# Kernel optimization log

Measured on AMD Instinct MI355X. Metric: run time of the kernel, lower is better.

## Reference

```python
import jax, jax.numpy as jnp
import numpy as np

B, S, E, H = 8, 2048, 512, 8
DH = E // H
NEG = -1e30


def setup_inputs() -> dict:
    key = jax.random.key(0)
    ks = jax.random.split(key, 6)
    return {
        "x": jax.random.normal(ks[0], (B, S, E), dtype=jnp.float32),
        "W_qkv": jax.random.normal(ks[1], (E, 3 * E), dtype=jnp.float32) * 0.02,
        "b_qkv": jax.random.normal(ks[2], (3 * E,), dtype=jnp.float32) * 0.02,
        "W_out": jax.random.normal(ks[3], (E, E), dtype=jnp.float32) * 0.02,
        "b_out": jax.random.normal(ks[4], (E,), dtype=jnp.float32) * 0.02,
        "rel_pos": jax.random.normal(ks[5], (1, H, S, S), dtype=jnp.float32) * 0.02,
    }


def reference(x, W_qkv, b_qkv, W_out, b_out, rel_pos):
    b, s, e = x.shape
    scale = DH ** -0.5
    qkv = x @ W_qkv + b_qkv                     # [b, s, 3e]
    qkv = qkv.reshape(b, s, 3, H, DH)
    q = jnp.transpose(qkv[:, :, 0], (0, 2, 1, 3))  # [b, h, s, dh]
    k = jnp.transpose(qkv[:, :, 1], (0, 2, 1, 3))
    v = jnp.transpose(qkv[:, :, 2], (0, 2, 1, 3))
    scores = jnp.einsum("bhqd,bhkd->bhqk", q, k) * scale
    scores = scores + rel_pos[:, :, :s, :s]
    causal = jnp.tril(jnp.ones((s, s), dtype=bool))
    scores = jnp.where(causal[None, None], scores, NEG)
    attn = jax.nn.softmax(scores, axis=-1)
    out = jnp.einsum("bhqk,bhkd->bhqd", attn, v)  # [b, h, s, dh]
    out = jnp.transpose(out, (0, 2, 1, 3)).reshape(b, s, e)
    return out @ W_out + b_out
```

## Files before the change

kernel.cpp:

```cpp
#include <hip/hip_runtime.h>
#include <cstdint>


#define DEVI __device__ __forceinline__

typedef __bf16 bf8 __attribute__((ext_vector_type(8)));
typedef float f4 __attribute__((ext_vector_type(4)));
typedef unsigned short us8 __attribute__((ext_vector_type(8)));
typedef unsigned short us4 __attribute__((ext_vector_type(4)));

typedef const unsigned int __attribute__((address_space(1))) gu32;
typedef unsigned int __attribute__((address_space(3))) lu32;

DEVI unsigned short f2bf(float f) {
  unsigned u = __builtin_bit_cast(unsigned, f);
  u += 0x7fffu + ((u >> 16) & 1u);
  return (unsigned short)(u >> 16);
}

DEVI void gl_lds16(const void* g, void* l) {
  __builtin_amdgcn_global_load_lds((gu32*)g, (lu32*)l, 16, 0, 0);
}

DEVI bf8 comb(us4 a, us4 b) {
  us8 r;
  r[0]=a[0]; r[1]=a[1]; r[2]=a[2]; r[3]=a[3];
  r[4]=b[0]; r[5]=b[1]; r[6]=b[2]; r[7]=b[3];
  return __builtin_bit_cast(bf8, r);
}

__global__ __launch_bounds__(256) void k_convert_x(const float* __restrict__ x,
                                                   unsigned short* __restrict__ xb) {
  int c = blockIdx.x * 256 + threadIdx.x;
  int row = c >> 6, cl = c & 63;
  const float* s = x + ((size_t)row << 9) + (cl << 3);
  float4 a = *(const float4*)s;
  float4 b = *(const float4*)(s + 4);
  us8 o;
  o[0]=f2bf(a.x); o[1]=f2bf(a.y); o[2]=f2bf(a.z); o[3]=f2bf(a.w);
  o[4]=f2bf(b.x); o[5]=f2bf(b.y); o[6]=f2bf(b.z); o[7]=f2bf(b.w);
  int p = (cl & ~7) | ((cl & 7) ^ (row & 7));
  *(us8*)(xb + ((size_t)row << 9) + (p << 3)) = o;
}

__global__ __launch_bounds__(256) void k_transpose_w(const float* __restrict__ W,
                                                     unsigned short* __restrict__ Wt, int N) {
  __shared__ float t[32][33];
  int k0 = blockIdx.x * 32, n0 = blockIdx.y * 32;
  int tx = threadIdx.x & 31, ty = threadIdx.x >> 5;
#pragma unroll
  for (int r = 0; r < 4; ++r)
    t[ty + r * 8][tx] = W[(size_t)(k0 + ty + r * 8) * N + n0 + tx];
  __syncthreads();
#pragma unroll
  for (int r = 0; r < 4; ++r) {
    int n = n0 + ty + r * 8, k = k0 + tx;
    int k2 = (k & ~63) | ((((k >> 3) & 7) ^ (n & 7)) << 3) | (k & 7);
    Wt[((size_t)n << 9) + k2] = f2bf(t[tx][ty + r * 8]);
  }
}

template <int EPI>
__global__ __launch_bounds__(256, 2)
void k_gemm(const unsigned short* __restrict__ Ag, const unsigned short* __restrict__ Bg,
            const float* __restrict__ bias, float* __restrict__ Of,
            unsigned short* __restrict__ Oq, unsigned short* __restrict__ Ok,
            unsigned short* __restrict__ Ov) {
  __shared__ __align__(16) unsigned short lds[128 * 64 * 2];
  unsigned short* Al = lds;
  unsigned short* Bl = lds + 128 * 64;
  const int tid = threadIdx.x, wv = tid >> 6, lane = tid & 63, g = lane >> 4, cl = lane & 15;
  const int wm = wv >> 1, wn = wv & 1;
  const int row0 = blockIdx.x * 128, col0 = blockIdx.y * 128;
  f4 acc[4][4];
#pragma unroll
  for (int i = 0; i < 4; ++i)
#pragma unroll
    for (int j = 0; j < 4; ++j) acc[i][j] = (f4){0.f, 0.f, 0.f, 0.f};

  for (int kt = 0; kt < 8; ++kt) {
#pragma unroll
    for (int j = 0; j < 4; ++j) {
      int ci = wv * 4 + j;
      int gci = ci * 64 + lane;
      int r = gci >> 3, cc = gci & 7;
      gl_lds16(Ag + ((size_t)(row0 + r) << 9) + kt * 64 + cc * 8, Al + ci * 512);
      gl_lds16(Bg + ((size_t)(col0 + r) << 9) + kt * 64 + cc * 8, Bl + ci * 512);
    }
    __syncthreads();
#pragma unroll
    for (int kk = 0; kk < 2; ++kk) {
      bf8 af[4], bb[4];
#pragma unroll
      for (int mf = 0; mf < 4; ++mf) {
        int r = wm * 64 + mf * 16 + cl;
        int cc = (kk * 4 + g) ^ (r & 7);
        af[mf] = *(const bf8*)(Al + r * 64 + cc * 8);
      }
#pragma unroll
      for (int nf = 0; nf < 4; ++nf) {
        int r = wn * 64 + nf * 16 + cl;
        int cc = (kk * 4 + g) ^ (r & 7);
        bb[nf] = *(const bf8*)(Bl + r * 64 + cc * 8);
      }
#pragma unroll
      for (int mf = 0; mf < 4; ++mf)
#pragma unroll
        for (int nf = 0; nf < 4; ++nf)
          acc[mf][nf] = __builtin_amdgcn_mfma_f32_16x16x32_bf16(af[mf], bb[nf], acc[mf][nf], 0, 0, 0);
    }
    __syncthreads();
  }

  if (EPI == 1) {
#pragma unroll
    for (int nf = 0; nf < 4; ++nf) {
      int col = col0 + wn * 64 + nf * 16 + cl;
      float bv = bias[col];
#pragma unroll
      for (int mf = 0; mf < 4; ++mf) {
#pragma unroll
        for (int j = 0; j < 4; ++j) {
          int row = row0 + wm * 64 + mf * 16 + 4 * g + j;
          Of[((size_t)row << 9) + col] = acc[mf][nf][j] + bv;
        }
      }
    }
  } else {
    const int which = col0 >> 9;
#pragma unroll
    for (int nf = 0; nf < 4; ++nf) {
      int col = col0 + wn * 64 + nf * 16 + cl;
      float bv = bias[col];
      int d = col & 63, h = (col >> 6) & 7;
#pragma unroll
      for (int mf = 0; mf < 4; ++mf) {
        int row = row0 + wm * 64 + mf * 16 + 4 * g;
        int b = row >> 11, s = row & 2047;
        size_t fb = ((size_t)b * 8 + h) * 131072;
        if (which == 0) {
#pragma unroll
          for (int j = 0; j < 4; ++j) {
            int ss = s + j;
            size_t off = fb + (size_t)((ss >> 4) * 1024 + (d >> 5) * 512 +
                                       (((d >> 3) & 3) * 16 + (ss & 15)) * 8 + (d & 7));
            Oq[off] = f2bf((acc[mf][nf][j] + bv) * 0.125f);
          }
        } else if (which == 1) {
#pragma unroll
          for (int j = 0; j < 4; ++j) {
            int ss = s + j;
            size_t off = fb + (size_t)((ss >> 6) * 4096 + (d >> 5) * 2048 + ((ss >> 4) & 3) * 512 +
                                       (((d >> 3) & 3) * 16 + (ss & 15)) * 8 + (d & 7));
            Ok[off] = f2bf(acc[mf][nf][j] + bv);
          }
        } else {
          us4 o;
#pragma unroll
          for (int j = 0; j < 4; ++j) o[j] = f2bf(acc[mf][nf][j] + bv);
          size_t off = fb + (size_t)((s >> 6) * 4096 + ((s >> 5) & 1) * 2048 + (d >> 4) * 512 +
                                     ((((s >> 3) & 3) * 16) + (d & 15)) * 8 + (s & 7));
          *(us4*)(Ov + off) = o;
        }
      }
    }
  }
}

__global__ __launch_bounds__(256, 3)
void k_attn(const unsigned short* __restrict__ Qf, const unsigned short* __restrict__ Kf,
            const unsigned short* __restrict__ Vf, const float* __restrict__ rel,
            unsigned short* __restrict__ AO) {
  __shared__ __align__(16) unsigned short Pl[4][16 * 68];
  const int tid = threadIdx.x, wv = tid >> 6, lane = tid & 63, g = lane >> 4, cl = lane & 15;
  int bid = blockIdx.x;
  int glo = bid & 7, rest = bid >> 3;
  int b = rest & 7, ghi = rest >> 3;
  int grp = ghi * 8 + glo;
  int h = grp >> 5, qt = 31 - (grp & 31);
  int qb = qt << 6;
  size_t fb = (((size_t)b << 3) + h) * 131072;
  const unsigned short* Qp = Qf + fb;
  const unsigned short* Kp = Kf + fb;
  const unsigned short* Vp = Vf + fb;
  const float* relp = rel + ((size_t)h << 22);
  const int qrb = qb + wv * 16;
  const int q16 = (qt << 2) + wv;

  bf8 qf[2];
#pragma unroll
  for (int kk = 0; kk < 2; ++kk)
    qf[kk] = *(const bf8*)(Qp + q16 * 1024 + kk * 512 + lane * 8);

  f4 oa[4];
  float mrun[4], lrun[4];
#pragma unroll
  for (int j = 0; j < 4; ++j) { mrun[j] = -1e30f; lrun[j] = 0.f; }
#pragma unroll
  for (int ct = 0; ct < 4; ++ct) oa[ct] = (f4){0.f, 0.f, 0.f, 0.f};

  unsigned short* pw = Pl[wv];

  for (int kt = 0; kt <= qt; ++kt) {
    int kb = kt << 6;
    const unsigned short* Kt = Kp + kt * 4096;
    const unsigned short* Vt = Vp + kt * 4096;
    bf8 kf[2][4], vf[2][4];
#pragma unroll
    for (int kk = 0; kk < 2; ++kk)
#pragma unroll
      for (int ct = 0; ct < 4; ++ct) {
        kf[kk][ct] = *(const bf8*)(Kt + kk * 2048 + ct * 512 + lane * 8);
        vf[kk][ct] = *(const bf8*)(Vt + kk * 2048 + ct * 512 + lane * 8);
      }
    float rl[4][4];
    const float* rb = relp + ((size_t)(qrb + 4 * g) << 11) + kb + cl;
#pragma unroll
    for (int ct = 0; ct < 4; ++ct)
#pragma unroll
      for (int j = 0; j < 4; ++j)
        rl[ct][j] = rb[(j << 11) + ct * 16];

    f4 sa[4];
#pragma unroll
    for (int ct = 0; ct < 4; ++ct) sa[ct] = (f4){0.f, 0.f, 0.f, 0.f};
#pragma unroll
    for (int kk = 0; kk < 2; ++kk)
#pragma unroll
      for (int ct = 0; ct < 4; ++ct)
        sa[ct] = __builtin_amdgcn_mfma_f32_16x16x32_bf16(qf[kk], kf[kk][ct], sa[ct], 0, 0, 0);

    if (kt == qt) {
#pragma unroll
      for (int ct = 0; ct < 4; ++ct) {
        int kcol = kb + ct * 16 + cl;
#pragma unroll
        for (int j = 0; j < 4; ++j) {
          int qrow = qrb + 4 * g + j;
          float sv = sa[ct][j] + rl[ct][j];
          sa[ct][j] = (kcol > qrow) ? -1e30f : sv;
        }
      }
    } else {
#pragma unroll
      for (int ct = 0; ct < 4; ++ct)
#pragma unroll
        for (int j = 0; j < 4; ++j) sa[ct][j] += rl[ct][j];
    }
    float al[4], mx[4];
#pragma unroll
    for (int j = 0; j < 4; ++j) {
      float m0 = fmaxf(fmaxf(sa[0][j], sa[1][j]), fmaxf(sa[2][j], sa[3][j]));
      m0 = fmaxf(m0, __shfl_xor(m0, 1, 16));
      m0 = fmaxf(m0, __shfl_xor(m0, 2, 16));
      m0 = fmaxf(m0, __shfl_xor(m0, 4, 16));
      m0 = fmaxf(m0, __shfl_xor(m0, 8, 16));
      float mn = fmaxf(mrun[j], m0);
      al[j] = __expf(mrun[j] - mn);
      mrun[j] = mn;
      mx[j] = mn;
    }
#pragma unroll
    for (int ct = 0; ct < 4; ++ct)
#pragma unroll
      for (int j = 0; j < 4; ++j) sa[ct][j] = __expf(sa[ct][j] - mx[j]);
#pragma unroll
    for (int j = 0; j < 4; ++j) {
      float rs = sa[0][j] + sa[1][j] + sa[2][j] + sa[3][j];
      rs += __shfl_xor(rs, 1, 16);
      rs += __shfl_xor(rs, 2, 16);
      rs += __shfl_xor(rs, 4, 16);
      rs += __shfl_xor(rs, 8, 16);
      lrun[j] = lrun[j] * al[j] + rs;
    }
#pragma unroll
    for (int ct = 0; ct < 4; ++ct) {
      oa[ct][0] *= al[0]; oa[ct][1] *= al[1]; oa[ct][2] *= al[2]; oa[ct][3] *= al[3];
    }
#pragma unroll
    for (int ct = 0; ct < 4; ++ct)
#pragma unroll
      for (int j = 0; j < 4; ++j)
        pw[(4 * g + j) * 68 + ct * 16 + cl] = f2bf(sa[ct][j]);
#pragma unroll
    for (int kk = 0; kk < 2; ++kk) {
      us4 p0 = *(const us4*)(pw + cl * 68 + kk * 32 + g * 8);
      us4 p1 = *(const us4*)(pw + cl * 68 + kk * 32 + g * 8 + 4);
      bf8 pf = comb(p0, p1);
#pragma unroll
      for (int ct = 0; ct < 4; ++ct)
        oa[ct] = __builtin_amdgcn_mfma_f32_16x16x32_bf16(pf, vf[kk][ct], oa[ct], 0, 0, 0);
    }
  }
#pragma unroll
  for (int j = 0; j < 4; ++j) {
    float inv = 1.0f / lrun[j];
    int s = qrb + 4 * g + j;
#pragma unroll
    for (int ct = 0; ct < 4; ++ct) {
      int d = ct * 16 + cl;
      int d2 = (d & 7) | (((d >> 3) ^ (s & 7)) << 3);
      AO[(((size_t)b << 11) + s) * 512 + h * 64 + d2] = f2bf(oa[ct][j] * inv);
    }
  }
}

extern "C" void kernel_launch(void* const* d_in, const int* in_sizes, int n_in,
                              void* d_out, int out_size, void* d_ws, size_t ws_size,
                              hipStream_t stream) {
  const float* x    = (const float*)d_in[0];
  const float* Wqkv = (const float*)d_in[1];
  const float* bqkv = (const float*)d_in[2];
  const float* Wout = (const float*)d_in[3];
  const float* bout = (const float*)d_in[4];
  const float* rel  = (const float*)d_in[5];
  float* out = (float*)d_out;

  unsigned short* Qw  = (unsigned short*)d_ws;
  unsigned short* Kw  = Qw  + 8388608;
  unsigned short* Vw  = Kw  + 8388608;
  unsigned short* AOw = Vw  + 8388608;
  unsigned short* Xb  = AOw + 8388608;
  unsigned short* WtQ = Xb  + 8388608;
  unsigned short* WtO = WtQ + 786432;

  k_convert_x<<<dim3(4096), dim3(256), 0, stream>>>(x, Xb);
  k_transpose_w<<<dim3(16, 48), dim3(256), 0, stream>>>(Wqkv, WtQ, 1536);
  k_transpose_w<<<dim3(16, 16), dim3(256), 0, stream>>>(Wout, WtO, 512);
  k_gemm<0><<<dim3(128, 12), dim3(256), 0, stream>>>(Xb, WtQ, bqkv, nullptr, Qw, Kw, Vw);
  k_attn<<<dim3(2048), dim3(256), 0, stream>>>(Qw, Kw, Vw, rel, AOw);
  k_gemm<1><<<dim3(128, 4), dim3(256), 0, stream>>>(AOw, WtO, bout, out, nullptr, nullptr, nullptr);
}
```

Baseline: 243.1 us.

## Process two query tiles per block sharing K/V loads; prelayout rel_pos as bf16

```diff
diff --git a/kernel.cpp b/kernel.cpp
--- a/kernel.cpp
+++ b/kernel.cpp
@@ -58,6 +58,21 @@
     int k2 = (k & ~63) | ((((k >> 3) & 7) ^ (n & 7)) << 3) | (k & 7);
     Wt[((size_t)n << 9) + k2] = f2bf(t[tx][ty + r * 8]);
   }
+}
+
+__global__ __launch_bounds__(256) void k_relconv(const float* __restrict__ rel,
+                                                 unsigned short* __restrict__ relt) {
+  int t = blockIdx.x * 256 + threadIdx.x;
+  int lane = t & 63, ct = (t >> 6) & 3, kt = (t >> 8) & 31, q16 = (t >> 13) & 127, h = t >> 20;
+  if (kt > (q16 >> 2)) return;
+  int row0 = (q16 << 4) + ((lane >> 4) << 2);
+  int col = (kt << 6) + (ct << 4) + (lane & 15);
+  const float* rp = rel + ((size_t)h << 22) + ((size_t)row0 << 11) + col;
+  us4 o;
+#pragma unroll
+  for (int j = 0; j < 4; ++j) o[j] = f2bf(rp[(size_t)j << 11]);
+  size_t idx = ((((((size_t)h << 7) | q16) << 5) | kt) << 2 | ct) << 6 | lane;
+  *(us4*)(relt + (idx << 2)) = o;
 }
 
 template <int EPI>
@@ -167,140 +182,169 @@
   }
 }
 
+DEVI void qk16(f4* sa, const bf8* qf_, const bf8 kf[2][4]) {
+#pragma unroll
+  for (int ct = 0; ct < 4; ++ct) sa[ct] = (f4){0.f, 0.f, 0.f, 0.f};
+#pragma unroll
+  for (int kk = 0; kk < 2; ++kk)
+#pragma unroll
+    for (int ct = 0; ct < 4; ++ct)
+      sa[ct] = __builtin_amdgcn_mfma_f32_16x16x32_bf16(qf_[kk], kf[kk][ct], sa[ct], 0, 0, 0);
+}
+
+template <bool RELT>
+DEVI void addrel16(f4* sa, const float* relp, const unsigned short* relt,
+                   int h, int q16X, int rX, int kt, int kb, int g, int cl, int lane) {
+  if constexpr (RELT) {
+    const unsigned short* tb = relt + (((((size_t)h << 7) | q16X) << 5) | kt) * 1024;
+#pragma unroll
+    for (int ct = 0; ct < 4; ++ct) {
+      us4 r = *(const us4*)(tb + ((ct << 6) | lane) * 4);
+#pragma unroll
+      for (int j = 0; j < 4; ++j)
+        sa[ct][j] += __builtin_bit_cast(float, (unsigned)r[j] << 16);
+    }
+  } else {
+    const float* rb = relp + ((size_t)(rX + 4 * g) << 11) + kb + cl;
+#pragma unroll
+    for (int ct = 0; ct < 4; ++ct)
+#pragma unroll
+      for (int j = 0; j < 4; ++j) sa[ct][j] += rb[((size_t)j << 11) + ct * 16];
+  }
+}
+
+DEVI void maskdiag(f4* sa, int rX, int kb, int g, int cl) {
+#pragma unroll
+  for (int ct = 0; ct < 4; ++ct) {
+    int kcol = kb + ct * 16 + cl;
+#pragma unroll
+    for (int j = 0; j < 4; ++j)
+      if (kcol > rX + 4 * g + j) sa[ct][j] = -1e30f;
+  }
+}
+
+DEVI void smpv16(f4* sa, f4* oa, float* mr, float* lr, const bf8 vf[2][4],
+                 unsigned short* pw, int g, int cl) {
+  float al[4], mx[4];
+#pragma unroll
+  for (int j = 0; j < 4; ++j) {
+    float m0 = fmaxf(fmaxf(sa[0][j], sa[1][j]), fmaxf(sa[2][j], sa[3][j]));
+    m0 = fmaxf(m0, __shfl_xor(m0, 1, 16));
+    m0 = fmaxf(m0, __shfl_xor(m0, 2, 16));
+    m0 = fmaxf(m0, __shfl_xor(m0, 4, 16));
+    m0 = fmaxf(m0, __shfl_xor(m0, 8, 16));
+    float mn = fmaxf(mr[j], m0);
+    al[j] = __expf(mr[j] - mn);
+    mr[j] = mn; mx[j] = mn;
+  }
+#pragma unroll
+  for (int ct = 0; ct < 4; ++ct)
+#pragma unroll
+    for (int j = 0; j < 4; ++j) sa[ct][j] = __expf(sa[ct][j] - mx[j]);
+#pragma unroll
+  for (int j = 0; j < 4; ++j) {
+    float rs = sa[0][j] + sa[1][j] + sa[2][j] + sa[3][j];
+    rs += __shfl_xor(rs, 1, 16);
+    rs += __shfl_xor(rs, 2, 16);
+    rs += __shfl_xor(rs, 4, 16);
+    rs += __shfl_xor(rs, 8, 16);
+    lr[j] = lr[j] * al[j] + rs;
+  }
+#pragma unroll
+  for (int ct = 0; ct < 4; ++ct) {
+    oa[ct][0] *= al[0]; oa[ct][1] *= al[1]; oa[ct][2] *= al[2]; oa[ct][3] *= al[3];
+  }
+#pragma unroll
+  for (int ct = 0; ct < 4; ++ct)
+#pragma unroll
+    for (int j = 0; j < 4; ++j)
+      pw[(4 * g + j) * 68 + ct * 16 + cl] = f2bf(sa[ct][j]);
+#pragma unroll
+  for (int kk = 0; kk < 2; ++kk) {
+    us4 p0 = *(const us4*)(pw + cl * 68 + kk * 32 + g * 8);
+    us4 p1 = *(const us4*)(pw + cl * 68 + kk * 32 + g * 8 + 4);
+    bf8 pf = comb(p0, p1);
+#pragma unroll
+    for (int ct = 0; ct < 4; ++ct)
+      oa[ct] = __builtin_amdgcn_mfma_f32_16x16x32_bf16(pf, vf[kk][ct], oa[ct], 0, 0, 0);
+  }
+}
+
+template <bool RELT>
 __global__ __launch_bounds__(256, 3)
 void k_attn(const unsigned short* __restrict__ Qf, const unsigned short* __restrict__ Kf,
             const unsigned short* __restrict__ Vf, const float* __restrict__ rel,
-            unsigned short* __restrict__ AO) {
+            const unsigned short* __restrict__ relt, unsigned short* __restrict__ AO) {
   __shared__ __align__(16) unsigned short Pl[4][16 * 68];
   const int tid = threadIdx.x, wv = tid >> 6, lane = tid & 63, g = lane >> 4, cl = lane & 15;
   int bid = blockIdx.x;
   int glo = bid & 7, rest = bid >> 3;
   int b = rest & 7, ghi = rest >> 3;
   int grp = ghi * 8 + glo;
-  int h = grp >> 5, qt = 31 - (grp & 31);
-  int qb = qt << 6;
+  int h = grp >> 4, qt2 = 15 - (grp & 15);
+  int qb2 = qt2 << 7;
   size_t fb = (((size_t)b << 3) + h) * 131072;
   const unsigned short* Qp = Qf + fb;
   const unsigned short* Kp = Kf + fb;
   const unsigned short* Vp = Vf + fb;
   const float* relp = rel + ((size_t)h << 22);
-  const int qrb = qb + wv * 16;
-  const int q16 = (qt << 2) + wv;
-
-  bf8 qf[2];
-#pragma unroll
-  for (int kk = 0; kk < 2; ++kk)
-    qf[kk] = *(const bf8*)(Qp + q16 * 1024 + kk * 512 + lane * 8);
-
-  f4 oa[4];
-  float mrun[4], lrun[4];
-#pragma unroll
-  for (int j = 0; j < 4; ++j) { mrun[j] = -1e30f; lrun[j] = 0.f; }
-#pragma unroll
-  for (int ct = 0; ct < 4; ++ct) oa[ct] = (f4){0.f, 0.f, 0.f, 0.f};
+  const int rA = qb2 + wv * 16, rB = rA + 64;
+  const int q16A = (qt2 << 3) + wv, q16B = q16A + 4;
+
+  bf8 qfA[2], qfB[2];
+#pragma unroll
+  for (int kk = 0; kk < 2; ++kk) {
+    qfA[kk] = *(const bf8*)(Qp + q16A * 1024 + kk * 512 + lane * 8);
+    qfB[kk] = *(const bf8*)(Qp + q16B * 1024 + kk * 512 + lane * 8);
+  }
+
+  f4 oaA[4], oaB[4];
+  float mA[4], lA[4], mB[4], lB[4];
+#pragma unroll
+  for (int j = 0; j < 4; ++j) { mA[j] = -1e30f; lA[j] = 0.f; mB[j] = -1e30f; lB[j] = 0.f; }
+#pragma unroll
+  for (int ct = 0; ct < 4; ++ct) { oaA[ct] = (f4){0.f,0.f,0.f,0.f}; oaB[ct] = (f4){0.f,0.f,0.f,0.f}; }
 
   unsigned short* pw = Pl[wv];
 
-  for (int kt = 0; kt <= qt; ++kt) {
-    int kb = kt << 6;
-    const unsigned short* Kt = Kp + kt * 4096;
-    const unsigned short* Vt = Vp + kt * 4096;
-    bf8 kf[2][4], vf[2][4];
-#pragma unroll
-    for (int kk = 0; kk < 2; ++kk)
-#pragma unroll
-      for (int ct = 0; ct < 4; ++ct) {
-        kf[kk][ct] = *(const bf8*)(Kt + kk * 2048 + ct * 512 + lane * 8);
-        vf[kk][ct] = *(const bf8*)(Vt + kk * 2048 + ct * 512 + lane * 8);
-      }
-    float rl[4][4];
-    const float* rb = relp + ((size_t)(qrb + 4 * g) << 11) + kb + cl;
-#pragma unroll
-    for (int ct = 0; ct < 4; ++ct)
-#pragma unroll
-      for (int j = 0; j < 4; ++j)
-        rl[ct][j] = rb[(j << 11) + ct * 16];
-
-    f4 sa[4];
-#pragma unroll
-    for (int ct = 0; ct < 4; ++ct) sa[ct] = (f4){0.f, 0.f, 0.f, 0.f};
-#pragma unroll
-    for (int kk = 0; kk < 2; ++kk)
-#pragma unroll
-      for (int ct = 0; ct < 4; ++ct)
-        sa[ct] = __builtin_amdgcn_mfma_f32_16x16x32_bf16(qf[kk], kf[kk][ct], sa[ct], 0, 0, 0);
-
-    if (kt == qt) {
-#pragma unroll
-      for (int ct = 0; ct < 4; ++ct) {
-        int kcol = kb + ct * 16 + cl;
-#pragma unroll
-        for (int j = 0; j < 4; ++j) {
-          int qrow = qrb + 4 * g + j;
-          float sv = sa[ct][j] + rl[ct][j];
-          sa[ct][j] = (kcol > qrow) ? -1e30f : sv;
-        }
-      }
-    } else {
-#pragma unroll
-      for (int ct = 0; ct < 4; ++ct)
-#pragma unroll
-        for (int j = 0; j < 4; ++j) sa[ct][j] += rl[ct][j];
-    }
-    float al[4], mx[4];
-#pragma unroll
-    for (int j = 0; j < 4; ++j) {
-      float m0 = fmaxf(fmaxf(sa[0][j], sa[1][j]), fmaxf(sa[2][j], sa[3][j]));
-      m0 = fmaxf(m0, __shfl_xor(m0, 1, 16));
-      m0 = fmaxf(m0, __shfl_xor(m0, 2, 16));
-      m0 = fmaxf(m0, __shfl_xor(m0, 4, 16));
-      m0 = fmaxf(m0, __shfl_xor(m0, 8, 16));
-      float mn = fmaxf(mrun[j], m0);
-      al[j] = __expf(mrun[j] - mn);
-      mrun[j] = mn;
-      mx[j] = mn;
-    }
-#pragma unroll
-    for (int ct = 0; ct < 4; ++ct)
-#pragma unroll
-      for (int j = 0; j < 4; ++j) sa[ct][j] = __expf(sa[ct][j] - mx[j]);
-#pragma unroll
-    for (int j = 0; j < 4; ++j) {
-      float rs = sa[0][j] + sa[1][j] + sa[2][j] + sa[3][j];
-      rs += __shfl_xor(rs, 1, 16);
-      rs += __shfl_xor(rs, 2, 16);
-      rs += __shfl_xor(rs, 4, 16);
-      rs += __shfl_xor(rs, 8, 16);
-      lrun[j] = lrun[j] * al[j] + rs;
-    }
-#pragma unroll
-    for (int ct = 0; ct < 4; ++ct) {
-      oa[ct][0] *= al[0]; oa[ct][1] *= al[1]; oa[ct][2] *= al[2]; oa[ct][3] *= al[3];
-    }
-#pragma unroll
-    for (int ct = 0; ct < 4; ++ct)
-#pragma unroll
-      for (int j = 0; j < 4; ++j)
-        pw[(4 * g + j) * 68 + ct * 16 + cl] = f2bf(sa[ct][j]);
-#pragma unroll
-    for (int kk = 0; kk < 2; ++kk) {
-      us4 p0 = *(const us4*)(pw + cl * 68 + kk * 32 + g * 8);
-      us4 p1 = *(const us4*)(pw + cl * 68 + kk * 32 + g * 8 + 4);
-      bf8 pf = comb(p0, p1);
-#pragma unroll
-      for (int ct = 0; ct < 4; ++ct)
-        oa[ct] = __builtin_amdgcn_mfma_f32_16x16x32_bf16(pf, vf[kk][ct], oa[ct], 0, 0, 0);
-    }
-  }
+#define TILE(KT, AON, ADIAG, BDIAG) do {                                          \
+    int kb_ = (KT) << 6;                                                          \
+    const unsigned short* Kt_ = Kp + (KT) * 4096;                                 \
+    const unsigned short* Vt_ = Vp + (KT) * 4096;                                 \
+    bf8 kf[2][4];                                                                 \
+    _Pragma("unroll") for (int kk = 0; kk < 2; ++kk)                              \
+      _Pragma("unroll") for (int ct = 0; ct < 4; ++ct)                            \
+        kf[kk][ct] = *(const bf8*)(Kt_ + kk * 2048 + ct * 512 + lane * 8);        \
+    f4 saA[4], saB[4];                                                            \
+    if (AON) qk16(saA, qfA, kf);                                                  \
+    qk16(saB, qfB, kf);                                                           \
+    if (AON) addrel16<RELT>(saA, relp, relt, h, q16A, rA, (KT), kb_, g, cl, lane);\
+    addrel16<RELT>(saB, relp, relt, h, q16B, rB, (KT), kb_, g, cl, lane);         \
+    if (ADIAG) maskdiag(saA, rA, kb_, g, cl);                                     \
+    if (BDIAG) maskdiag(saB, rB, kb_, g, cl);                                     \
+    bf8 vf[2][4];                                                                 \
+    _Pragma("unroll") for (int kk = 0; kk < 2; ++kk)                              \
+      _Pragma("unroll") for (int ct = 0; ct < 4; ++ct)                            \
+        vf[kk][ct] = *(const bf8*)(Vt_ + kk * 2048 + ct * 512 + lane * 8);        \
+    if (AON) smpv16(saA, oaA, mA, lA, vf, pw, g, cl);                             \
+    smpv16(saB, oaB, mB, lB, vf, pw, g, cl);                                      \
+  } while (0)
+
+  for (int kt = 0; kt < 2 * qt2; ++kt) TILE(kt, true, false, false);
+  TILE(2 * qt2, true, true, false);
+  TILE(2 * qt2 + 1, false, false, true);
+#undef TILE
+
 #pragma unroll
   for (int j = 0; j < 4; ++j) {
-    float inv = 1.0f / lrun[j];
-    int s = qrb + 4 * g + j;
+    float invA = 1.0f / lA[j], invB = 1.0f / lB[j];
+    int sA_ = rA + 4 * g + j, sB_ = rB + 4 * g + j;
 #pragma unroll
     for (int ct = 0; ct < 4; ++ct) {
       int d = ct * 16 + cl;
-      int d2 = (d & 7) | (((d >> 3) ^ (s & 7)) << 3);
-      AO[(((size_t)b << 11) + s) * 512 + h * 64 + d2] = f2bf(oa[ct][j] * inv);
+      int d2 = (d & 7) | (((d >> 3) ^ (sA_ & 7)) << 3);
+      AO[(((size_t)b << 11) + sA_) * 512 + h * 64 + d2] = f2bf(oaA[ct][j] * invA);
+      AO[(((size_t)b << 11) + sB_) * 512 + h * 64 + d2] = f2bf(oaB[ct][j] * invB);
     }
   }
 }
@@ -319,15 +363,18 @@
   unsigned short* Qw  = (unsigned short*)d_ws;
   unsigned short* Kw  = Qw  + 8388608;
   unsigned short* Vw  = Kw  + 8388608;
-  unsigned short* AOw = Vw  + 8388608;
-  unsigned short* Xb  = AOw + 8388608;
-  unsigned short* WtQ = Xb  + 8388608;
+  unsigned short* XA  = Vw  + 8388608;
+  unsigned short* WtQ = XA  + 8388608;
   unsigned short* WtO = WtQ + 786432;
-
-  k_convert_x<<<dim3(4096), dim3(256), 0, stream>>>(x, Xb);
+  unsigned short* relt= WtO + 262144;
+  const bool useT = ws_size >= (34603008ULL + 33554432ULL) * 2ULL;
+
+  k_convert_x<<<dim3(4096), dim3(256), 0, stream>>>(x, XA);
   k_transpose_w<<<dim3(16, 48), dim3(256), 0, stream>>>(Wqkv, WtQ, 1536);
   k_transpose_w<<<dim3(16, 16), dim3(256), 0, stream>>>(Wout, WtO, 512);
-  k_gemm<0><<<dim3(128, 12), dim3(256), 0, stream>>>(Xb, WtQ, bqkv, nullptr, Qw, Kw, Vw);
-  k_attn<<<dim3(2048), dim3(256), 0, stream>>>(Qw, Kw, Vw, rel, AOw);
-  k_gemm<1><<<dim3(128, 4), dim3(256), 0, stream>>>(AOw, WtO, bout, out, nullptr, nullptr, nullptr);
-}
+  if (useT) k_relconv<<<dim3(32768), dim3(256), 0, stream>>>(rel, relt);
+  k_gemm<0><<<dim3(128, 12), dim3(256), 0, stream>>>(XA, WtQ, bqkv, nullptr, Qw, Kw, Vw);
+  if (useT) k_attn<true ><<<dim3(1024), dim3(256), 0, stream>>>(Qw, Kw, Vw, rel, relt, XA);
+  else      k_attn<false><<<dim3(1024), dim3(256), 0, stream>>>(Qw, Kw, Vw, rel, relt, XA);
+  k_gemm<1><<<dim3(128, 4), dim3(256), 0, stream>>>(XA, WtO, bout, out, nullptr, nullptr, nullptr);
+}
```

New measurement: 279.1 us. 14.8% more time.
